# Kernel tuning notes

Measured on AMD Instinct MI355X. Metric: run time of the kernel, lower is better.

## Reference

```python
import jax, jax.numpy as jnp
import numpy as np

NUM_CLASSES = 21
TOP_K = 200
CONF_THRESH = 0.01
NMS_THRESH = 0.45
VAR0, VAR1 = 0.1, 0.2
B, P = 64, 8732  # SSD300 VOC prior count


def setup_inputs() -> dict:
    key = jax.random.key(0)
    k1, k2, k3 = jax.random.split(key, 3)
    loc = jax.random.normal(k1, (B, P, 4), dtype=jnp.float32)
    conf = jax.random.normal(k2, (B, P, NUM_CLASSES), dtype=jnp.float32)
    priors = jax.random.uniform(k3, (P, 4), dtype=jnp.float32, minval=0.02, maxval=1.0)
    return {"loc": loc, "conf": conf, "priors": priors}


def _decode(loc, priors):
    # loc, priors: [P, 4] (cx, cy, w, h) offsets -> corner boxes [P, 4]
    cxcy = priors[:, :2] + loc[:, :2] * VAR0 * priors[:, 2:]
    wh = priors[:, 2:] * jnp.exp(loc[:, 2:] * VAR1)
    x1y1 = cxcy - wh * 0.5
    x2y2 = x1y1 + wh
    return jnp.concatenate([x1y1, x2y2], axis=1)


def _iou_matrix(boxes):
    # boxes [K,4] -> pairwise IoU [K,K] with the original +1 pixel convention
    x1, y1, x2, y2 = boxes[:, 0], boxes[:, 1], boxes[:, 2], boxes[:, 3]
    area = (x2 - x1 + 1.0) * (y2 - y1 + 1.0)
    xx1 = jnp.maximum(x1[:, None], x1[None, :])
    yy1 = jnp.maximum(y1[:, None], y1[None, :])
    xx2 = jnp.minimum(x2[:, None], x2[None, :])
    yy2 = jnp.minimum(y2[:, None], y2[None, :])
    w = jnp.maximum(0.0, xx2 - xx1 + 1.0)
    h = jnp.maximum(0.0, yy2 - yy1 + 1.0)
    inter = w * h
    return inter / (area[:, None] + area[None, :] - inter)


def _nms_keep(boxes, valid):
    # boxes [K,4] sorted by descending score; greedy NMS as a fixed-length loop
    K = boxes.shape[0]
    iou = _iou_matrix(boxes)
    later = jnp.arange(K)[None, :] > jnp.arange(K)[:, None]  # strictly lower-priority

    def body(i, suppressed):
        keep_i = valid[i] & ~suppressed[i]
        return suppressed | (keep_i & (iou[i] > NMS_THRESH) & later[i])

    suppressed = jax.lax.fori_loop(0, K, body, jnp.zeros((K,), bool))
    return valid & ~suppressed


def _per_class(scores, decoded):
    # scores [P], decoded [P,4] -> [TOP_K, 7] rows (score, x1, y1, x2, y2, 0, 0)
    valid_p = scores > CONF_THRESH
    s = jnp.where(valid_p, scores, -1.0)
    top_s, idx = jax.lax.top_k(s, TOP_K)
    b = decoded[idx]                      # [K,4]
    valid = top_s > CONF_THRESH
    keep = _nms_keep(b, valid)
    rows = jnp.concatenate([top_s[:, None], b], axis=1)  # [K,5]
    order = jnp.argsort(~keep)            # stable: kept rows compacted to front
    rows = jnp.where(keep[order][:, None], rows[order], 0.0)
    return jnp.pad(rows, ((0, 0), (0, 2)))  # pad to width 7 (original leaves cols 5:7 zero)


def _per_image(loc_i, conf_i, priors):
    decoded = _decode(loc_i, priors)      # [P,4]
    # classes 1..C-1 (skip background class 0)
    cls_scores = conf_i[:, 1:].T          # [C-1, P]
    cls_out = jax.vmap(lambda s: _per_class(s, decoded))(cls_scores)  # [C-1,K,7]
    bg = jnp.zeros((1, TOP_K, 7), dtype=loc_i.dtype)
    return jnp.concatenate([bg, cls_out], axis=0)  # [C,K,7]


def _detect(loc, conf, priors):
    conf_soft = jax.nn.softmax(conf, axis=-1)  # SSD test phase applies softmax
    output = jax.vmap(_per_image, in_axes=(0, 0, None))(loc, conf_soft, priors)  # [B,C,K,7]
    flt = output.reshape(output.shape[0], -1, 7)  # [B, C*K, 7]
    score = flt[:, :, 0]
    idx = jnp.argsort(-score, axis=1)
    rank = jnp.argsort(idx, axis=1)
    mask = rank < TOP_K
    order = jnp.argsort(~mask, axis=1)    # stable: top-K rows, original positional order
    sel = jnp.take_along_axis(flt, order[:, :TOP_K, None], axis=1)  # [B,K,7]
    return sel.reshape(-1, 7)             # [B*K, 7], matching flt[rank < top_k]


def reference(loc, conf, priors):
    return _detect(loc, conf, priors)
```

## Files before the change

### kernel.cpp

```cpp
#include <hip/hip_runtime.h>
#include <stdint.h>

#define NUM_P 8732
#define NUM_B 64
#define NUM_CLS 21
#define TOPK 200
#define NMS_T 0.45f
#define CONF_T 0.01f
#define NL 35
#define NV4 2183
#define NL2 16
#define MAXCAND 4000
#define ORD_SENT 0x407FFFFFu
#define HI_BITS 0x17800u

__device__ __forceinline__ uint32_t ordf(float f) {
    uint32_t u = __float_as_uint(f);
    return (u & 0x80000000u) ? ~u : (u | 0x80000000u);
}
__device__ __forceinline__ float unordf(uint32_t v) {
    uint32_t u = (v & 0x80000000u) ? (v ^ 0x80000000u) : ~v;
    return __uint_as_float(u);
}

__global__ __launch_bounds__(256) void prep_kernel(const float* __restrict__ conf,
                                                   uint32_t* __restrict__ ct,
                                                   uint32_t* __restrict__ candCount) {
    __shared__ float tile[256 * NUM_CLS];
    const int bx = blockIdx.x;
    const int b = blockIdx.y;
    const int tid = threadIdx.x;
    if (bx == 0 && b == 0 && tid < NUM_B) candCount[tid] = 0u;
    const int p0 = bx * 256;
    const int np = min(256, NUM_P - p0);
    const int nf4 = (np * NUM_CLS) / 4;
    const float4* src = reinterpret_cast<const float4*>(conf + ((size_t)b * NUM_P + p0) * NUM_CLS);
    float4* dst = reinterpret_cast<float4*>(tile);
#pragma unroll
    for (int i = 0; i < 6; ++i) {
        int idx = tid + i * 256;
        if (idx < nf4) dst[idx] = src[idx];
    }
    __syncthreads();
    if (tid < np) {
        const int p = p0 + tid;
        const float* row = tile + tid * NUM_CLS;
        float x[NUM_CLS];
#pragma unroll
        for (int c = 0; c < NUM_CLS; ++c) x[c] = row[c];
        float m = x[0];
#pragma unroll
        for (int c = 1; c < NUM_CLS; ++c) m = fmaxf(m, x[c]);
        float e[NUM_CLS];
        float s = 0.0f;
#pragma unroll
        for (int c = 0; c < NUM_CLS; ++c) { e[c] = expf(x[c] - m); s += e[c]; }
#pragma unroll
        for (int c = 1; c < NUM_CLS; ++c) {
            float sc = e[c] / s;
            float sv = (sc > CONF_T) ? sc : -1.0f;
            ct[((size_t)(b * 20 + (c - 1))) * NUM_P + p] = ordf(sv);
        }
    }
}

__global__ __launch_bounds__(256) void select_kernel(const uint32_t* __restrict__ ct,
                                                     const float* __restrict__ loc,
                                                     const float* __restrict__ priors,
                                                     float* __restrict__ selS,
                                                     float* __restrict__ selX1,
                                                     float* __restrict__ selY1,
                                                     float* __restrict__ selX2,
                                                     float* __restrict__ selY2) {
    __shared__ uint32_t hist[2048];
    __shared__ uint32_t wtot[4];
    __shared__ uint32_t sh_d, sh_above, sh_bnd, sh_nsent;
    __shared__ uint64_t skey[256];
    __shared__ int scnt;
    __shared__ int sh_run;

    const int blk = blockIdx.x;
    const int b = blk / 20;
    const int tid = threadIdx.x;
    const int lane = tid & 63;
    const int wv = tid >> 6;
    const uint32_t* col = ct + (size_t)blk * NUM_P;
    const uint4* colv = reinterpret_cast<const uint4*>(col);

#pragma unroll
    for (int i = 0; i < 8; ++i) hist[tid + i * 256] = 0;
    skey[tid] = 0;
    if (tid == 0) { scnt = 0; sh_run = 0; }
    __syncthreads();

    int nsent = 0;
#pragma unroll
    for (int i = 0; i < 9; ++i) {
        int idx = tid + i * 256;
        if (idx < NV4) {
            uint4 v = colv[idx];
            uint32_t a0 = v.x, a1 = v.y, a2 = v.z, a3 = v.w;
            if (a0 == ORD_SENT) nsent++; else atomicAdd(&hist[(a0 >> 15) & 2047u], 1u);
            if (a1 == ORD_SENT) nsent++; else atomicAdd(&hist[(a1 >> 15) & 2047u], 1u);
            if (a2 == ORD_SENT) nsent++; else atomicAdd(&hist[(a2 >> 15) & 2047u], 1u);
            if (a3 == ORD_SENT) nsent++; else atomicAdd(&hist[(a3 >> 15) & 2047u], 1u);
        }
    }
    {
        int v = nsent;
#pragma unroll
        for (int off = 32; off; off >>= 1) v += __shfl_down(v, off);
        if (lane == 0) wtot[wv] = (uint32_t)v;
        __syncthreads();
        if (tid == 0) sh_nsent = wtot[0] + wtot[1] + wtot[2] + wtot[3];
        __syncthreads();
    }
    const int nreal = NUM_P - (int)sh_nsent;

    uint32_t emitThr = 0;
    bool ranked = false;
    uint32_t thrEq = 0;
    int needEq = 0;

    if (nreal >= TOPK) {
        {
            const int tbase = tid * 8;
            uint32_t ls = 0;
#pragma unroll
            for (int j = 0; j < 8; ++j) ls += hist[tbase + j];
            uint32_t v = ls;
#pragma unroll
            for (int off = 1; off < 64; off <<= 1) {
                uint32_t o2 = __shfl_down(v, off);
                if (lane + off < 64) v += o2;
            }
            if (lane == 0) wtot[wv] = v;
            __syncthreads();
            uint32_t above_wave = 0;
            for (int w = wv + 1; w < 4; ++w) above_wave += wtot[w];
            uint32_t acc = (v + above_wave) - ls;
            for (int j = 7; j >= 0; --j) {
                uint32_t h = hist[tbase + j];
                if (acc < (uint32_t)TOPK && acc + h >= (uint32_t)TOPK) {
                    sh_d = (uint32_t)(tbase + j);
                    sh_above = acc;
                    sh_bnd = h;
                }
                acc += h;
            }
            __syncthreads();
        }
        uint32_t d1 = sh_d;
        int cert = (int)sh_above;
        int need = TOPK - cert;
        int bnd = (int)sh_bnd;
        const uint32_t lvl1 = HI_BITS | d1;

        if (cert + bnd <= 256) {
            emitThr = lvl1 << 15;
        } else {
            __syncthreads();
#pragma unroll
            for (int i = 0; i < 8; ++i) hist[tid + i * 256] = 0;
            __syncthreads();
#pragma unroll
            for (int i = 0; i < 9; ++i) {
                int idx = tid + i * 256;
                if (idx < NV4) {
                    uint4 v = colv[idx];
                    if ((v.x >> 15) == lvl1) atomicAdd(&hist[(v.x >> 4) & 2047u], 1u);
                    if ((v.y >> 15) == lvl1) atomicAdd(&hist[(v.y >> 4) & 2047u], 1u);
                    if ((v.z >> 15) == lvl1) atomicAdd(&hist[(v.z >> 4) & 2047u], 1u);
                    if ((v.w >> 15) == lvl1) atomicAdd(&hist[(v.w >> 4) & 2047u], 1u);
                }
            }
            __syncthreads();
            {
                const int tbase = tid * 8;
                uint32_t ls = 0;
#pragma unroll
                for (int j = 0; j < 8; ++j) ls += hist[tbase + j];
                uint32_t v = ls;
#pragma unroll
                for (int off = 1; off < 64; off <<= 1) {
                    uint32_t o2 = __shfl_down(v, off);
                    if (lane + off < 64) v += o2;
                }
                if (lane == 0) wtot[wv] = v;
                __syncthreads();
                uint32_t above_wave = 0;
                for (int w = wv + 1; w < 4; ++w) above_wave += wtot[w];
                uint32_t acc = (v + above_wave) - ls;
                for (int j = 7; j >= 0; --j) {
                    uint32_t h = hist[tbase + j];
                    if (acc < (uint32_t)need && acc + h >= (uint32_t)need) {
                        sh_d = (uint32_t)(tbase + j);
                        sh_above = acc;
                        sh_bnd = h;
                    }
                    acc += h;
                }
                __syncthreads();
            }
            uint32_t d2 = sh_d;
            cert += (int)sh_above;
            need -= (int)sh_above;
            bnd = (int)sh_bnd;
            const uint32_t pfx28 = (lvl1 << 11) | d2;

            if (cert + bnd <= 256) {
                emitThr = pfx28 << 4;
            } else {
                __syncthreads();
                if (tid < 16) hist[tid] = 0;
                __syncthreads();
#pragma unroll
                for (int i = 0; i < 9; ++i) {
                    int idx = tid + i * 256;
                    if (idx < NV4) {
                        uint4 v = colv[idx];
                        if ((v.x >> 4) == pfx28) atomicAdd(&hist[v.x & 15u], 1u);
                        if ((v.y >> 4) == pfx28) atomicAdd(&hist[v.y & 15u], 1u);
                        if ((v.z >> 4) == pfx28) atomicAdd(&hist[v.z & 15u], 1u);
                        if ((v.w >> 4) == pfx28) atomicAdd(&hist[v.w & 15u], 1u);
                    }
                }
                __syncthreads();
                if (tid == 0) {
                    uint32_t acc = 0;
                    for (int j = 15; j >= 0; --j) {
                        uint32_t h = hist[j];
                        if (acc < (uint32_t)need && acc + h >= (uint32_t)need) {
                            sh_d = (uint32_t)j; sh_above = acc; sh_bnd = h; break;
                        }
                        acc += h;
                    }
                }
                __syncthreads();
                uint32_t d3 = sh_d;
                cert += (int)sh_above;
                need -= (int)sh_above;
                bnd = (int)sh_bnd;
                const uint32_t pfx32 = (pfx28 << 4) | d3;
                if (cert + bnd <= 256) {
                    emitThr = pfx32;
                } else {
                    ranked = true; thrEq = pfx32; needEq = need;
                }
            }
        }
    } else {
        ranked = true; thrEq = ORD_SENT; needEq = TOPK - nreal;
    }

    if (!ranked) {
#pragma unroll
        for (int i = 0; i < 9; ++i) {
            int idx = tid + i * 256;
            if (idx < NV4) {
                uint4 v = colv[idx];
                uint32_t aa[4] = {v.x, v.y, v.z, v.w};
#pragma unroll
                for (int j = 0; j < 4; ++j) {
                    uint32_t o = aa[j];
                    if (o >= emitThr) {
                        int s0 = atomicAdd(&scnt, 1);
                        uint32_t p = (uint32_t)(idx * 4 + j);
                        if (s0 < 256)
                            skey[s0] = ((uint64_t)o << 32) | (0xFFFFFFFFu - p);
                    }
                }
            }
        }
        __syncthreads();
    } else {
        for (int i = 0; i < NL; ++i) {
            int p = i * 256 + tid;
            uint32_t o = (p < NUM_P) ? col[p] : 0u;
            if (o > thrEq) {
                int s0 = atomicAdd(&scnt, 1);
                if (s0 < 256)
                    skey[s0] = ((uint64_t)o << 32) | (0xFFFFFFFFu - (uint32_t)p);
            }
            bool tie = (p < NUM_P) && (o == thrEq);
            unsigned long long ball = __ballot(tie);
            if (lane == 0) wtot[wv] = (uint32_t)__popcll(ball);
            __syncthreads();
            int rank = sh_run;
            for (int w = 0; w < wv; ++w) rank += (int)wtot[w];
            rank += __popcll(ball & ((1ull << lane) - 1ull));
            if (tie && rank < needEq) {
                int s0 = atomicAdd(&scnt, 1);
                if (s0 < 256)
                    skey[s0] = ((uint64_t)o << 32) | (0xFFFFFFFFu - (uint32_t)p);
            }
            __syncthreads();
            if (tid == 0) sh_run += (int)(wtot[0] + wtot[1] + wtot[2] + wtot[3]);
            __syncthreads();
        }
    }

    for (int k = 2; k <= 256; k <<= 1) {
        for (int j = k >> 1; j > 0; j >>= 1) {
            int ixj = tid ^ j;
            if (ixj > tid) {
                uint64_t a = skey[tid], bb = skey[ixj];
                bool up = (tid & k) == 0;
                bool sw = up ? (a < bb) : (a > bb);
                if (sw) { skey[tid] = bb; skey[ixj] = a; }
            }
            __syncthreads();
        }
    }

    if (tid < TOPK) {
        uint64_t k = skey[tid];
        uint32_t p = 0xFFFFFFFFu - (uint32_t)k;
        float msc = unordf((uint32_t)(k >> 32));
        const float4 l4 = reinterpret_cast<const float4*>(loc)[(size_t)b * NUM_P + p];
        const float4 pr = reinterpret_cast<const float4*>(priors)[p];
        float cx = pr.x + (l4.x * 0.1f) * pr.z;
        float cy = pr.y + (l4.y * 0.1f) * pr.w;
        float w  = pr.z * expf(l4.z * 0.2f);
        float h  = pr.w * expf(l4.w * 0.2f);
        float mx1 = cx - w * 0.5f;
        float my1 = cy - h * 0.5f;
        float mx2 = mx1 + w;
        float my2 = my1 + h;
        size_t o0 = (size_t)blk * TOPK + tid;
        selS[o0] = msc; selX1[o0] = mx1; selY1[o0] = my1; selX2[o0] = mx2; selY2[o0] = my2;
    }
}

__global__ __launch_bounds__(64) void nms_kernel(float* __restrict__ selS,
                                                 float* __restrict__ selX1,
                                                 float* __restrict__ selY1,
                                                 float* __restrict__ selX2,
                                                 float* __restrict__ selY2,
                                                 uint64_t* __restrict__ cands,
                                                 uint32_t* __restrict__ candCount) {
    const int blk = blockIdx.x;
    const int b = blk / 20;
    const int c = blk % 20;
    const int lane = threadIdx.x;
    const size_t base = (size_t)blk * TOPK;

    float scs[4], x1s[4], y1s[4], x2s[4], y2s[4], ars[4];
    uint32_t validm = 0, supm = 0;
#pragma unroll
    for (int s = 0; s < 4; ++s) {
        int idx = s * 64 + lane;
        bool v = idx < TOPK;
        scs[s] = v ? selS[base + idx] : -1.0f;
        x1s[s] = v ? selX1[base + idx] : 0.0f;
        y1s[s] = v ? selY1[base + idx] : 0.0f;
        x2s[s] = v ? selX2[base + idx] : 0.0f;
        y2s[s] = v ? selY2[base + idx] : 0.0f;
        ars[s] = (x2s[s] - x1s[s] + 1.0f) * (y2s[s] - y1s[s] + 1.0f);
        if (v && scs[s] > CONF_T) validm |= (1u << s);
    }

#pragma unroll
    for (int slot = 0; slot < 4; ++slot) {
        const int nown = (slot == 3) ? (TOPK - 3 * 64) : 64;
        for (int owner = 0; owner < nown; ++owner) {
            const int i = slot * 64 + owner;
            int myk = (int)((validm >> slot) & 1u) & (int)(((supm >> slot) & 1u) ^ 1u);
            int keep_i = __shfl(myk, owner);
            if (keep_i) {
                float bx1 = __shfl(x1s[slot], owner);
                float by1 = __shfl(y1s[slot], owner);
                float bx2 = __shfl(x2s[slot], owner);
                float by2 = __shfl(y2s[slot], owner);
                float bar_ = __shfl(ars[slot], owner);
#pragma unroll
                for (int s2 = 0; s2 < 4; ++s2) {
                    int idx = s2 * 64 + lane;
                    if (idx > i && idx < TOPK) {
                        float xx1 = fmaxf(bx1, x1s[s2]);
                        float yy1 = fmaxf(by1, y1s[s2]);
                        float xx2 = fminf(bx2, x2s[s2]);
                        float yy2 = fminf(by2, y2s[s2]);
                        float w = fmaxf(0.0f, xx2 - xx1 + 1.0f);
                        float h = fmaxf(0.0f, yy2 - yy1 + 1.0f);
                        float inter = w * h;
                        float iou = inter / (bar_ + ars[s2] - inter);
                        if (iou > NMS_T) supm |= (1u << s2);
                    }
                }
            }
        }
    }

    int off = 0;
    uint64_t wkey[4];
    int wrank[4];
    bool wk[4];
#pragma unroll
    for (int s = 0; s < 4; ++s) {
        int idx = s * 64 + lane;
        bool kept = (idx < TOPK) && ((validm >> s) & 1u) && !((supm >> s) & 1u);
        unsigned long long ball = __ballot(kept);
        int rank = off + __popcll(ball & ((1ull << lane) - 1ull));
        wk[s] = kept;
        wrank[s] = rank;
        wkey[s] = 0;
        if (kept) {
            selS[base + rank] = scs[s];
            selX1[base + rank] = x1s[s];
            selY1[base + rank] = y1s[s];
            selX2[base + rank] = x2s[s];
            selY2[base + rank] = y2s[s];
            uint32_t pos = (uint32_t)(c + 1) * TOPK + (uint32_t)rank;
            wkey[s] = ((uint64_t)ordf(scs[s]) << 32) | (uint32_t)(0xFFFFFFFFu - pos);
        }
        off += __popcll(ball);
    }
    uint32_t bcast = 0;
    if (lane == 0) bcast = atomicAdd(&candCount[b], (uint32_t)off);
    bcast = (uint32_t)__shfl((int)bcast, 0);
#pragma unroll
    for (int s = 0; s < 4; ++s)
        if (wk[s]) cands[(size_t)b * MAXCAND + bcast + wrank[s]] = wkey[s];
}

__global__ __launch_bounds__(256) void final_kernel(const uint64_t* __restrict__ cands,
                                                    const uint32_t* __restrict__ candCount,
                                                    const float* __restrict__ selS,
                                                    const float* __restrict__ selX1,
                                                    const float* __restrict__ selY1,
                                                    const float* __restrict__ selX2,
                                                    const float* __restrict__ selY2,
                                                    float* __restrict__ out) {
    const int b = blockIdx.x;
    const int tid = threadIdx.x;
    const int lane = tid & 63;
    const int wv = tid >> 6;
    const int n = (int)candCount[b];

    uint64_t key[NL2];
#pragma unroll
    for (int i = 0; i < NL2; ++i) {
        int idx = tid + i * 256;
        key[i] = (idx < n) ? cands[(size_t)b * MAXCAND + idx] : 0ull;
    }

    __shared__ int wsum[2][4];
    uint64_t prefix = 0;
    if (n > TOPK) {
        for (int bit = 63; bit >= 0; --bit) {
            uint64_t cand = prefix | (1ull << bit);
            int cnt = 0;
#pragma unroll
            for (int i = 0; i < NL2; ++i) cnt += (key[i] >= cand) ? 1 : 0;
            for (int off = 32; off; off >>= 1) cnt += __shfl_down(cnt, off);
            int bufi = bit & 1;
            if (lane == 0) wsum[bufi][wv] = cnt;
            __syncthreads();
            int tot = wsum[bufi][0] + wsum[bufi][1] + wsum[bufi][2] + wsum[bufi][3];
            if (tot >= TOPK) prefix = cand;
        }
    }

    __shared__ uint32_t selpos[256];
    __shared__ int scnt;
    selpos[tid] = 0xFFFFFFFFu;
    if (tid == 0) scnt = 0;
    __syncthreads();
#pragma unroll
    for (int i = 0; i < NL2; ++i)
        if (key[i] != 0ull && key[i] >= prefix) {
            int s = atomicAdd(&scnt, 1);
            selpos[s] = 0xFFFFFFFFu - (uint32_t)key[i];
        }
    __syncthreads();
    int nsel = scnt;

    for (int k = 2; k <= 256; k <<= 1) {
        for (int j = k >> 1; j > 0; j >>= 1) {
            int ixj = tid ^ j;
            if (ixj > tid) {
                uint32_t a = selpos[tid], bb = selpos[ixj];
                bool up = (tid & k) == 0;
                bool sw = up ? (a > bb) : (a < bb);
                if (sw) { selpos[tid] = bb; selpos[ixj] = a; }
            }
            __syncthreads();
        }
    }

    if (tid < TOPK) {
        int T = TOPK - (nsel < TOPK ? nsel : TOPK);
        float* o = out + ((size_t)b * TOPK + tid) * 7;
        if (tid < T) {
            o[0] = 0.f; o[1] = 0.f; o[2] = 0.f; o[3] = 0.f; o[4] = 0.f; o[5] = 0.f; o[6] = 0.f;
        } else {
            uint32_t pos = selpos[tid - T];
            uint32_t cc = pos / TOPK;
            uint32_t sl = pos % TOPK;
            size_t r = ((size_t)b * 20 + (cc - 1)) * TOPK + sl;
            o[0] = selS[r]; o[1] = selX1[r]; o[2] = selY1[r]; o[3] = selX2[r]; o[4] = selY2[r];
            o[5] = 0.f; o[6] = 0.f;
        }
    }
}

extern "C" void kernel_launch(void* const* d_in, const int* in_sizes, int n_in,
                              void* d_out, int out_size, void* d_ws, size_t ws_size,
                              hipStream_t stream) {
    const float* loc    = (const float*)d_in[0];
    const float* conf   = (const float*)d_in[1];
    const float* priors = (const float*)d_in[2];
    float* out = (float*)d_out;

    const size_t CAND_BYTES = (size_t)NUM_B * MAXCAND * sizeof(uint64_t);
    const size_t SEL_ONE    = (size_t)NUM_B * 20 * TOPK * sizeof(float);
    const size_t CNT_BYTES  = 256;

    char* ws = (char*)d_ws;
    uint64_t* cands     = (uint64_t*)ws;
    float*    selS      = (float*)(ws + CAND_BYTES);
    float*    selX1     = (float*)(ws + CAND_BYTES + SEL_ONE);
    float*    selY1     = (float*)(ws + CAND_BYTES + 2 * SEL_ONE);
    float*    selX2     = (float*)(ws + CAND_BYTES + 3 * SEL_ONE);
    float*    selY2     = (float*)(ws + CAND_BYTES + 4 * SEL_ONE);
    uint32_t* candCount = (uint32_t*)(ws + CAND_BYTES + 5 * SEL_ONE);
    uint32_t* ct        = (uint32_t*)(ws + CAND_BYTES + 5 * SEL_ONE + CNT_BYTES);

    dim3 pgrid((NUM_P + 255) / 256, NUM_B);
    prep_kernel<<<pgrid, 256, 0, stream>>>(conf, ct, candCount);
    select_kernel<<<NUM_B * 20, 256, 0, stream>>>(ct, loc, priors,
                                                  selS, selX1, selY1, selX2, selY2);
    nms_kernel<<<NUM_B * 20, 64, 0, stream>>>(selS, selX1, selY1, selX2, selY2,
                                              cands, candCount);
    final_kernel<<<NUM_B, 256, 0, stream>>>(cands, candCount,
                                            selS, selX1, selY1, selX2, selY2, out);
}
```

Before: 79.45 us.

## Fuse top-k selection and NMS into one kernel, cache column in registers

```diff
diff --git a/kernel.cpp b/kernel.cpp
--- a/kernel.cpp
+++ b/kernel.cpp
@@ -64,14 +64,16 @@
     }
 }
 
-__global__ __launch_bounds__(256) void select_kernel(const uint32_t* __restrict__ ct,
-                                                     const float* __restrict__ loc,
-                                                     const float* __restrict__ priors,
-                                                     float* __restrict__ selS,
-                                                     float* __restrict__ selX1,
-                                                     float* __restrict__ selY1,
-                                                     float* __restrict__ selX2,
-                                                     float* __restrict__ selY2) {
+__global__ __launch_bounds__(256, 4) void select_nms_kernel(const uint32_t* __restrict__ ct,
+                                                            const float* __restrict__ loc,
+                                                            const float* __restrict__ priors,
+                                                            float* __restrict__ selS,
+                                                            float* __restrict__ selX1,
+                                                            float* __restrict__ selY1,
+                                                            float* __restrict__ selX2,
+                                                            float* __restrict__ selY2,
+                                                            uint64_t* __restrict__ cands,
+                                                            uint32_t* __restrict__ candCount) {
     __shared__ uint32_t hist[2048];
     __shared__ uint32_t wtot[4];
     __shared__ uint32_t sh_d, sh_above, sh_bnd, sh_nsent;
@@ -81,6 +83,7 @@
 
     const int blk = blockIdx.x;
     const int b = blk / 20;
+    const int c = blk % 20;
     const int tid = threadIdx.x;
     const int lane = tid & 63;
     const int wv = tid >> 6;
@@ -93,13 +96,19 @@
     if (tid == 0) { scnt = 0; sh_run = 0; }
     __syncthreads();
 
+    uint4 vv[9];
+#pragma unroll
+    for (int i = 0; i < 9; ++i) {
+        int idx = tid + i * 256;
+        vv[i] = make_uint4(ORD_SENT, ORD_SENT, ORD_SENT, ORD_SENT);
+        if (idx < NV4) vv[i] = colv[idx];
+    }
     int nsent = 0;
 #pragma unroll
     for (int i = 0; i < 9; ++i) {
         int idx = tid + i * 256;
         if (idx < NV4) {
-            uint4 v = colv[idx];
-            uint32_t a0 = v.x, a1 = v.y, a2 = v.z, a3 = v.w;
+            uint32_t a0 = vv[i].x, a1 = vv[i].y, a2 = vv[i].z, a3 = vv[i].w;
             if (a0 == ORD_SENT) nsent++; else atomicAdd(&hist[(a0 >> 15) & 2047u], 1u);
             if (a1 == ORD_SENT) nsent++; else atomicAdd(&hist[(a1 >> 15) & 2047u], 1u);
             if (a2 == ORD_SENT) nsent++; else atomicAdd(&hist[(a2 >> 15) & 2047u], 1u);
@@ -167,11 +176,10 @@
             for (int i = 0; i < 9; ++i) {
                 int idx = tid + i * 256;
                 if (idx < NV4) {
-                    uint4 v = colv[idx];
-                    if ((v.x >> 15) == lvl1) atomicAdd(&hist[(v.x >> 4) & 2047u], 1u);
-                    if ((v.y >> 15) == lvl1) atomicAdd(&hist[(v.y >> 4) & 2047u], 1u);
-                    if ((v.z >> 15) == lvl1) atomicAdd(&hist[(v.z >> 4) & 2047u], 1u);
-                    if ((v.w >> 15) == lvl1) atomicAdd(&hist[(v.w >> 4) & 2047u], 1u);
+                    if ((vv[i].x >> 15) == lvl1) atomicAdd(&hist[(vv[i].x >> 4) & 2047u], 1u);
+                    if ((vv[i].y >> 15) == lvl1) atomicAdd(&hist[(vv[i].y >> 4) & 2047u], 1u);
+                    if ((vv[i].z >> 15) == lvl1) atomicAdd(&hist[(vv[i].z >> 4) & 2047u], 1u);
+                    if ((vv[i].w >> 15) == lvl1) atomicAdd(&hist[(vv[i].w >> 4) & 2047u], 1u);
                 }
             }
             __syncthreads();
@@ -218,11 +226,10 @@
                 for (int i = 0; i < 9; ++i) {
                     int idx = tid + i * 256;
                     if (idx < NV4) {
-                        uint4 v = colv[idx];
-                        if ((v.x >> 4) == pfx28) atomicAdd(&hist[v.x & 15u], 1u);
-                        if ((v.y >> 4) == pfx28) atomicAdd(&hist[v.y & 15u], 1u);
-                        if ((v.z >> 4) == pfx28) atomicAdd(&hist[v.z & 15u], 1u);
-                        if ((v.w >> 4) == pfx28) atomicAdd(&hist[v.w & 15u], 1u);
+                        if ((vv[i].x >> 4) == pfx28) atomicAdd(&hist[vv[i].x & 15u], 1u);
+                        if ((vv[i].y >> 4) == pfx28) atomicAdd(&hist[vv[i].y & 15u], 1u);
+                        if ((vv[i].z >> 4) == pfx28) atomicAdd(&hist[vv[i].z & 15u], 1u);
+                        if ((vv[i].w >> 4) == pfx28) atomicAdd(&hist[vv[i].w & 15u], 1u);
                     }
                 }
                 __syncthreads();
@@ -258,8 +265,7 @@
         for (int i = 0; i < 9; ++i) {
             int idx = tid + i * 256;
             if (idx < NV4) {
-                uint4 v = colv[idx];
-                uint32_t aa[4] = {v.x, v.y, v.z, v.w};
+                uint32_t aa[4] = {vv[i].x, vv[i].y, vv[i].z, vv[i].w};
 #pragma unroll
                 for (int j = 0; j < 4; ++j) {
                     uint32_t o = aa[j];
@@ -313,6 +319,13 @@
         }
     }
 
+    float* nb = reinterpret_cast<float*>(hist);
+    float* dsc = nb;
+    float* dx1 = nb + TOPK;
+    float* dy1 = nb + 2 * TOPK;
+    float* dx2 = nb + 3 * TOPK;
+    float* dy2 = nb + 4 * TOPK;
+    float* dar = nb + 5 * TOPK;
     if (tid < TOPK) {
         uint64_t k = skey[tid];
         uint32_t p = 0xFFFFFFFFu - (uint32_t)k;
@@ -327,23 +340,11 @@
         float my1 = cy - h * 0.5f;
         float mx2 = mx1 + w;
         float my2 = my1 + h;
-        size_t o0 = (size_t)blk * TOPK + tid;
-        selS[o0] = msc; selX1[o0] = mx1; selY1[o0] = my1; selX2[o0] = mx2; selY2[o0] = my2;
-    }
-}
-
-__global__ __launch_bounds__(64) void nms_kernel(float* __restrict__ selS,
-                                                 float* __restrict__ selX1,
-                                                 float* __restrict__ selY1,
-                                                 float* __restrict__ selX2,
-                                                 float* __restrict__ selY2,
-                                                 uint64_t* __restrict__ cands,
-                                                 uint32_t* __restrict__ candCount) {
-    const int blk = blockIdx.x;
-    const int b = blk / 20;
-    const int c = blk % 20;
-    const int lane = threadIdx.x;
-    const size_t base = (size_t)blk * TOPK;
+        dsc[tid] = msc; dx1[tid] = mx1; dy1[tid] = my1; dx2[tid] = mx2; dy2[tid] = my2;
+        dar[tid] = (mx2 - mx1 + 1.0f) * (my2 - my1 + 1.0f);
+    }
+    __syncthreads();
+    if (wv != 0) return;
 
     float scs[4], x1s[4], y1s[4], x2s[4], y2s[4], ars[4];
     uint32_t validm = 0, supm = 0;
@@ -351,12 +352,12 @@
     for (int s = 0; s < 4; ++s) {
         int idx = s * 64 + lane;
         bool v = idx < TOPK;
-        scs[s] = v ? selS[base + idx] : -1.0f;
-        x1s[s] = v ? selX1[base + idx] : 0.0f;
-        y1s[s] = v ? selY1[base + idx] : 0.0f;
-        x2s[s] = v ? selX2[base + idx] : 0.0f;
-        y2s[s] = v ? selY2[base + idx] : 0.0f;
-        ars[s] = (x2s[s] - x1s[s] + 1.0f) * (y2s[s] - y1s[s] + 1.0f);
+        scs[s] = v ? dsc[idx] : -1.0f;
+        x1s[s] = v ? dx1[idx] : 0.0f;
+        y1s[s] = v ? dy1[idx] : 0.0f;
+        x2s[s] = v ? dx2[idx] : 0.0f;
+        y2s[s] = v ? dy2[idx] : 0.0f;
+        ars[s] = v ? dar[idx] : 1.0f;
         if (v && scs[s] > CONF_T) validm |= (1u << s);
     }
 
@@ -392,6 +393,7 @@
         }
     }
 
+    const size_t base = (size_t)blk * TOPK;
     int off = 0;
     uint64_t wkey[4];
     int wrank[4];
@@ -529,10 +531,9 @@
 
     dim3 pgrid((NUM_P + 255) / 256, NUM_B);
     prep_kernel<<<pgrid, 256, 0, stream>>>(conf, ct, candCount);
-    select_kernel<<<NUM_B * 20, 256, 0, stream>>>(ct, loc, priors,
-                                                  selS, selX1, selY1, selX2, selY2);
-    nms_kernel<<<NUM_B * 20, 64, 0, stream>>>(selS, selX1, selY1, selX2, selY2,
-                                              cands, candCount);
+    select_nms_kernel<<<NUM_B * 20, 256, 0, stream>>>(ct, loc, priors,
+                                                      selS, selX1, selY1, selX2, selY2,
+                                                      cands, candCount);
     final_kernel<<<NUM_B, 256, 0, stream>>>(cands, candCount,
                                             selS, selX1, selY1, selX2, selY2, out);
 }
```

New measurement: 69.99 us. 11.9% less time.
